# Optimization experiments

Hardware: AMD Instinct MI355X
Metric: run time of the kernel (lower is better)

The kernel has to match this reference:

```python
import jax, jax.numpy as jnp
import numpy as np

L = 2          # conv layers
N = 50000      # nodes
E = 800000     # edges (before self loops)
F_IN = 256     # raw node features
C = 32         # embed features (out_channels per head)
H = 4          # heads
HC = H * C
ED = 1         # edge feature dim
EPS = 1e-5
NEG_SLOPE = 0.2


def _xavier(k, shape):
    fan_in, fan_out = shape[-2], shape[-1]
    lim = float(np.sqrt(6.0 / (fan_in + fan_out)))
    return jax.random.uniform(k, shape, jnp.float32, -lim, lim)


def setup_inputs() -> dict:
    key = jax.random.key(0)
    ks = jax.random.split(key, 12)
    x = jax.random.normal(ks[0], (N, F_IN), jnp.float32)
    src = jax.random.randint(ks[1], (E,), 0, N, dtype=jnp.int32)
    off = jax.random.randint(ks[2], (E,), 1, N, dtype=jnp.int32)
    dst = (src + off) % N  # guarantees no pre-existing self loops (PyG removes then re-adds them)
    edge_index = jnp.stack([src, dst])
    edge_attr = jax.random.normal(ks[3], (E, ED), jnp.float32)
    return {
        "x": x,
        "edge_index": edge_index,
        "edge_attr": edge_attr,
        "W_emb": _xavier(ks[4], (F_IN, C)),
        "b_emb": jnp.zeros((C,), jnp.float32),
        "ln0_w": jnp.ones((C,), jnp.float32),
        "ln0_b": jnp.zeros((C,), jnp.float32),
        "Wl": _xavier(ks[5], (L, C, HC)),
        "bl": jnp.zeros((L, HC), jnp.float32),
        "Wr": _xavier(ks[6], (L, C, HC)),
        "br": jnp.zeros((L, HC), jnp.float32),
        "We": _xavier(ks[7], (L, ED, HC)),
        "att": jax.random.normal(ks[8], (L, H, C), jnp.float32) * 0.1,
        "gat_b": jnp.zeros((L, HC), jnp.float32),
        "ln1_w": jnp.ones((L, HC), jnp.float32),
        "ln1_b": jnp.zeros((L, HC), jnp.float32),
        "lin_w": _xavier(ks[9], (L, HC, C)),
        "lin_b": jnp.zeros((L, C), jnp.float32),
        "ln2_w": jnp.ones((L, C), jnp.float32),
        "ln2_b": jnp.zeros((L, C), jnp.float32),
    }


def _node_ln(x, w, b):
    # torch.nn.LayerNorm over last dim
    mu = jnp.mean(x, axis=-1, keepdims=True)
    xc = x - mu
    var = jnp.mean(xc * xc, axis=-1, keepdims=True)
    return xc / jnp.sqrt(var + EPS) * w + b


def _graph_ln(x, w, b):
    # torch_geometric.nn.norm.LayerNorm, mode='graph': normalize over ALL nodes+features
    mu = jnp.mean(x)
    xc = x - mu
    var = jnp.mean(xc * xc)
    return xc / jnp.sqrt(var + EPS) * w + b


def _gatv2_layer(h, src, dst, ea, Wl, bl, Wr, br, We, att, gat_b):
    n = h.shape[0]
    xl = (h @ Wl + bl).reshape(n, H, C)   # lin_l(x) -> source transform
    xr = (h @ Wr + br).reshape(n, H, C)   # lin_r(x) -> target transform
    e = (ea @ We).reshape(-1, H, C)       # lin_edge(edge_attr), no bias
    z = jax.nn.leaky_relu(xl[src] + xr[dst] + e, NEG_SLOPE)   # [Etot,H,C]
    logits = jnp.einsum("ehc,hc->eh", z, att)                  # [Etot,H]
    # segment softmax over destination nodes (every node has a self loop)
    m = jax.ops.segment_max(logits, dst, num_segments=n)
    ex = jnp.exp(logits - m[dst])
    s = jax.ops.segment_sum(ex, dst, num_segments=n)
    alpha = ex / s[dst]                                        # [Etot,H]
    msg = alpha[..., None] * xl[src]                           # [Etot,H,C]
    out = jax.ops.segment_sum(msg, dst, num_segments=n)        # [N,H,C]
    return out.reshape(n, HC) + gat_b


def reference(x, edge_index, edge_attr, W_emb, b_emb, ln0_w, ln0_b, Wl, bl, Wr, br,
              We, att, gat_b, ln1_w, ln1_b, lin_w, lin_b, ln2_w, ln2_b):
    n = x.shape[0]
    loop = jnp.arange(n, dtype=edge_index.dtype)
    src = jnp.concatenate([edge_index[0], loop])
    dst = jnp.concatenate([edge_index[1], loop])
    ea = jnp.concatenate([edge_attr, jnp.zeros((n, edge_attr.shape[1]), edge_attr.dtype)])  # fill_value=0.0

    # node_embed: Dropout(eval=identity) -> Linear -> LayerNorm -> ReLU
    h = jax.nn.relu(_node_ln(x @ W_emb + b_emb, ln0_w, ln0_b))
    hs = [h]
    for i in range(L):
        g = _gatv2_layer(h, src, dst, ea, Wl[i], bl[i], Wr[i], br[i], We[i], att[i], gat_b[i])
        g = jax.nn.relu(_graph_ln(g, ln1_w[i], ln1_b[i]))     # PyG graph-mode LayerNorm + ReLU
        g = g @ lin_w[i] + lin_b[i]                            # heads>1 projection back to C
        h = jax.nn.relu(_node_ln(g, ln2_w[i], ln2_b[i]))
        hs.append(h)
    # JumpingKnowledge mode='max': elementwise max over layer outputs
    return jnp.max(jnp.stack(hs, axis=0), axis=0)
```

## Files before the change

### kernel.cpp

```cpp
#include <hip/hip_runtime.h>
#include <hip/hip_fp16.h>

constexpr int kNodes = 50000;
constexpr int kNE    = 800000;
constexpr int kFin   = 256;
constexpr int kC     = 32;
constexpr int kH     = 4;
constexpr int kHC    = 128;
constexpr int kTN    = 16;
constexpr int kWPh   = 264;
constexpr int kLWP   = 130;
constexpr int kEmbedBlocks = kNodes / kTN;
constexpr int kHistBlocks  = (kNE + 255) / 256;
constexpr int kTransBlocks = (kNodes + 31) / 32;
constexpr float kEps   = 1e-5f;
constexpr float kSlope = 0.2f;
constexpr float kL2E   = 1.44269504f;
constexpr float kShift2 = 8.0f * 1.44269504f;

typedef _Float16 f16;
typedef _Float16 f16x2 __attribute__((ext_vector_type(2)));
struct alignas(16) h8 { f16x2 v[4]; };

__device__ __forceinline__ float fdot2_(f16x2 a, f16x2 b, float c) {
#if __has_builtin(__builtin_amdgcn_fdot2)
    return __builtin_amdgcn_fdot2(a, b, c, false);
#else
    return fmaf((float)a.x, (float)b.x, fmaf((float)a.y, (float)b.y, c));
#endif
}

template<int CTRL>
__device__ __forceinline__ float dpp_add(float v) {
    int x = __builtin_amdgcn_update_dpp(0, __float_as_int(v), CTRL, 0xF, 0xF, true);
    return v + __int_as_float(x);
}
__device__ __forceinline__ float red8(float p) {
    p = dpp_add<0xB1>(p);
    p = dpp_add<0x4E>(p);
    p = dpp_add<0x141>(p);
    return p;
}

__global__ void __launch_bounds__(256) k_fill0(unsigned* __restrict__ p, int n) {
    int i = blockIdx.x * 256 + threadIdx.x;
    if (i < n) p[i] = 0u;
}

__global__ void __launch_bounds__(256) k_embed_hist(
    const float* __restrict__ x, const float* __restrict__ W, const float* __restrict__ b,
    const float* __restrict__ lnw, const float* __restrict__ lnb,
    float* __restrict__ h, float* __restrict__ jk,
    const int* __restrict__ dst, int* __restrict__ deg, unsigned short* __restrict__ rank) {
    __shared__ f16 sxh[kTN * kFin];
    __shared__ f16 sWh[kC * kWPh];
    int t = threadIdx.x;
    if (blockIdx.x < kHistBlocks) {
        int e = blockIdx.x * 256 + t;
        if (e < kNE) {
            int r = atomicAdd(&deg[dst[e]], 1);
            rank[e] = (unsigned short)r;
        }
        return;
    }
    int n0 = (blockIdx.x - kHistBlocks) * kTN;
    for (int i = t; i < kFin * kC; i += 256) {
        int k = i >> 5, c = i & 31;
        sWh[c * kWPh + k] = (f16)W[i];
    }
    const float2* xg2 = (const float2*)(x + (long)n0 * kFin);
    f16x2* sx2 = (f16x2*)sxh;
    for (int i = t; i < kTN * kFin / 2; i += 256) {
        float2 v = xg2[i];
        f16x2 hv; hv.x = (f16)v.x; hv.y = (f16)v.y;
        sx2[i] = hv;
    }
    __syncthreads();
    int c = t & 31, n2 = t >> 5;
    const h8* xa = (const h8*)(sxh + n2 * kFin);
    const h8* xb = (const h8*)(sxh + (n2 + 8) * kFin);
    const h8* wr = (const h8*)(sWh + c * kWPh);
    float a0 = 0.f, a0b = 0.f, a1 = 0.f, a1b = 0.f;
    #pragma unroll 8
    for (int i8 = 0; i8 < kFin / 8; ++i8) {
        h8 xv0 = xa[i8];
        h8 xv1 = xb[i8];
        h8 wv  = wr[i8];
        a0  = fdot2_(xv0.v[0], wv.v[0], a0);
        a0b = fdot2_(xv0.v[1], wv.v[1], a0b);
        a0  = fdot2_(xv0.v[2], wv.v[2], a0);
        a0b = fdot2_(xv0.v[3], wv.v[3], a0b);
        a1  = fdot2_(xv1.v[0], wv.v[0], a1);
        a1b = fdot2_(xv1.v[1], wv.v[1], a1b);
        a1  = fdot2_(xv1.v[2], wv.v[2], a1);
        a1b = fdot2_(xv1.v[3], wv.v[3], a1b);
    }
    float acc0 = a0 + a0b, acc1 = a1 + a1b;
    float bc = b[c], lw = lnw[c], lb = lnb[c];
    {
        float y = acc0 + bc;
        float m = y;
        #pragma unroll
        for (int o = 1; o < 32; o <<= 1) m += __shfl_xor(m, o);
        m *= (1.f / kC);
        float xc = y - m, v = xc * xc;
        #pragma unroll
        for (int o = 1; o < 32; o <<= 1) v += __shfl_xor(v, o);
        v *= (1.f / kC);
        float out = fmaxf(xc * rsqrtf(v + kEps) * lw + lb, 0.f);
        int node = n0 + n2;
        h[node * kC + c] = out;
        jk[node * kC + c] = out;
    }
    {
        float y = acc1 + bc;
        float m = y;
        #pragma unroll
        for (int o = 1; o < 32; o <<= 1) m += __shfl_xor(m, o);
        m *= (1.f / kC);
        float xc = y - m, v = xc * xc;
        #pragma unroll
        for (int o = 1; o < 32; o <<= 1) v += __shfl_xor(v, o);
        v *= (1.f / kC);
        float out = fmaxf(xc * rsqrtf(v + kEps) * lw + lb, 0.f);
        int node = n0 + n2 + 8;
        h[node * kC + c] = out;
        jk[node * kC + c] = out;
    }
}

__device__ __forceinline__ void trans_body(
    int bid, float* s_h, const float* __restrict__ h,
    const float* __restrict__ Wl, const float* __restrict__ bl,
    const float* __restrict__ Wr, const float* __restrict__ br,
    __half* __restrict__ xl, float* __restrict__ xr) {
    int t = threadIdx.x;
    int j = t & 127, hf = t >> 7;
    float wl[kC], wr[kC];
    #pragma unroll
    for (int k = 0; k < kC; ++k) { wl[k] = Wl[k * kHC + j]; wr[k] = Wr[k * kHC + j]; }
    float blj = bl[j], brj = br[j];
    int n0 = bid * 32;
    int nn = min(32, kNodes - n0);
    for (int i = t; i < nn * kC; i += 256) s_h[i] = h[n0 * kC + i];
    __syncthreads();
    int nend = min(nn, hf * 16 + 16);
    for (int n = hf * 16; n < nend; ++n) {
        const float4* h4 = (const float4*)(s_h + n * kC);
        float al = blj, ar = brj;
        #pragma unroll
        for (int kq = 0; kq < 8; ++kq) {
            float4 hv = h4[kq];
            al += hv.x * wl[kq*4] + hv.y * wl[kq*4+1] + hv.z * wl[kq*4+2] + hv.w * wl[kq*4+3];
            ar += hv.x * wr[kq*4] + hv.y * wr[kq*4+1] + hv.z * wr[kq*4+2] + hv.w * wr[kq*4+3];
        }
        long g = (long)(n0 + n) * kHC + j;
        xl[g] = __float2half(al);
        xr[g] = ar;
    }
}

__global__ void __launch_bounds__(256) k_trans(
    const float* __restrict__ h,
    const float* __restrict__ Wl, const float* __restrict__ bl,
    const float* __restrict__ Wr, const float* __restrict__ br,
    __half* __restrict__ xl, float* __restrict__ xr) {
    __shared__ float s_h[32 * kC];
    trans_body(blockIdx.x, s_h, h, Wl, bl, Wr, br, xl, xr);
}

__global__ void __launch_bounds__(256) k_trans_reorder(
    const float* __restrict__ h,
    const float* __restrict__ Wl, const float* __restrict__ bl,
    const float* __restrict__ Wr, const float* __restrict__ br,
    __half* __restrict__ xl, float* __restrict__ xr,
    const int* __restrict__ src, const int* __restrict__ dst, const float* __restrict__ ea,
    const int* __restrict__ rowptr, const unsigned short* __restrict__ rank,
    int2* __restrict__ epack) {
    __shared__ float s_h[32 * kC];
    if (blockIdx.x < kHistBlocks) {
        int e = blockIdx.x * 256 + threadIdx.x;
        if (e < kNE) {
            int d = dst[e];
            int pos = rowptr[d] + (int)rank[e];
            epack[pos] = make_int2(src[e], __float_as_int(ea[e]));
        }
        return;
    }
    trans_body(blockIdx.x - kHistBlocks, s_h, h, Wl, bl, Wr, br, xl, xr);
}

__global__ void __launch_bounds__(256) k_scan1(const int* __restrict__ deg,
                                               int* __restrict__ excl, int* __restrict__ bsum) {
    __shared__ int s[256];
    int t = threadIdx.x;
    int i = blockIdx.x * 256 + t;
    int v = (i < kNodes) ? deg[i] : 0;
    s[t] = v;
    __syncthreads();
    for (int o = 1; o < 256; o <<= 1) {
        int tv = (t >= o) ? s[t - o] : 0;
        __syncthreads();
        s[t] += tv;
        __syncthreads();
    }
    if (i < kNodes) excl[i] = s[t] - v;
    if (t == 255) bsum[blockIdx.x] = s[255];
}

__global__ void __launch_bounds__(256) k_scan2(int* __restrict__ bsum, int nb) {
    __shared__ int s[256];
    int t = threadIdx.x;
    int v = (t < nb) ? bsum[t] : 0;
    s[t] = v;
    __syncthreads();
    for (int o = 1; o < 256; o <<= 1) {
        int tv = (t >= o) ? s[t - o] : 0;
        __syncthreads();
        s[t] += tv;
        __syncthreads();
    }
    if (t < nb) bsum[t] = s[t];
}

__global__ void __launch_bounds__(256) k_scan3(int* __restrict__ excl, const int* __restrict__ bsum) {
    int i = blockIdx.x * 256 + threadIdx.x;
    if (i >= kNodes) return;
    if (blockIdx.x > 0) excl[i] += bsum[blockIdx.x - 1];
}

__global__ void __launch_bounds__(256) k_edge(
    const int* __restrict__ rowptr, const int* __restrict__ deg,
    const int2* __restrict__ epack,
    const __half* __restrict__ xl, float* __restrict__ xrg,
    const float* __restrict__ We, const float* __restrict__ att,
    const float* __restrict__ gat_b, float* __restrict__ ps, float* __restrict__ pq) {
    struct h4 { __half2 a, b; };
    int t = threadIdx.x & 63;
    int w = __builtin_amdgcn_readfirstlane(threadIdx.x >> 6);
    int d = blockIdx.x * 4 + w;
    int f = t & 31;
    bool slot0 = (t < 32);
    float em0 = slot0 ? 1.f : 0.f;

    const h4* xl4 = (const h4*)xl;
    long rowq = (long)d * 32;

    float4 xrv = ((const float4*)xrg)[rowq + f];
    float4 Wev = ((const float4*)We)[f];
    float4 av  = ((const float4*)att)[f];
    av.x *= kL2E; av.y *= kL2E; av.z *= kL2E; av.w *= kL2E;
    float4 gb  = ((const float4*)gat_b)[f];

    h4 xs = xl4[rowq + f];
    float2 xs01 = __half22float2(xs.a), xs23 = __half22float2(xs.b);

    float z0 = xs01.x + xrv.x, z1 = xs01.y + xrv.y;
    float z2 = xs23.x + xrv.z, z3 = xs23.y + xrv.w;
    z0 = fmaxf(z0, kSlope * z0); z1 = fmaxf(z1, kSlope * z1);
    z2 = fmaxf(z2, kSlope * z2); z3 = fmaxf(z3, kSlope * z3);
    float p = red8(z0 * av.x + z1 * av.y + z2 * av.z + z3 * av.w);
    float ee = __builtin_amdgcn_exp2f(p - kShift2) * em0;
    float l = ee;
    float o0 = ee * xs01.x, o1 = ee * xs01.y, o2 = ee * xs23.x, o3 = ee * xs23.y;

    int base = rowptr[d], cnt = deg[d];
    int npair = cnt >> 1;
    int e = 0;
    for (; e + 4 <= npair; e += 4) {
        int2 pa[4], pb[4];
        #pragma unroll
        for (int u = 0; u < 4; ++u) {
            pa[u] = epack[base + 2 * (e + u)];
            pb[u] = epack[base + 2 * (e + u) + 1];
        }
        h4 xv[4]; float eav[4];
        #pragma unroll
        for (int u = 0; u < 4; ++u) {
            int srow = slot0 ? pa[u].x : pb[u].x;
            xv[u] = xl4[(long)srow * 32 + f];
            eav[u] = __int_as_float(slot0 ? pa[u].y : pb[u].y);
        }
        #pragma unroll
        for (int u = 0; u < 4; ++u) {
            float2 x01 = __half22float2(xv[u].a), x23 = __half22float2(xv[u].b);
            float a0 = fmaf(eav[u], Wev.x, xrv.x) + x01.x;
            float a1 = fmaf(eav[u], Wev.y, xrv.y) + x01.y;
            float a2 = fmaf(eav[u], Wev.z, xrv.z) + x23.x;
            float a3 = fmaf(eav[u], Wev.w, xrv.w) + x23.y;
            a0 = fmaxf(a0, kSlope * a0); a1 = fmaxf(a1, kSlope * a1);
            a2 = fmaxf(a2, kSlope * a2); a3 = fmaxf(a3, kSlope * a3);
            float pp = red8(a0 * av.x + a1 * av.y + a2 * av.z + a3 * av.w);
            float eu = __builtin_amdgcn_exp2f(pp - kShift2);
            l += eu;
            o0 = fmaf(eu, x01.x, o0); o1 = fmaf(eu, x01.y, o1);
            o2 = fmaf(eu, x23.x, o2); o3 = fmaf(eu, x23.y, o3);
        }
    }
    for (; e < npair; ++e) {
        int2 pa = epack[base + 2 * e];
        int2 pb = epack[base + 2 * e + 1];
        int srow = slot0 ? pa.x : pb.x;
        float eav = __int_as_float(slot0 ? pa.y : pb.y);
        h4 xv = xl4[(long)srow * 32 + f];
        float2 x01 = __half22float2(xv.a), x23 = __half22float2(xv.b);
        float a0 = fmaf(eav, Wev.x, xrv.x) + x01.x;
        float a1 = fmaf(eav, Wev.y, xrv.y) + x01.y;
        float a2 = fmaf(eav, Wev.z, xrv.z) + x23.x;
        float a3 = fmaf(eav, Wev.w, xrv.w) + x23.y;
        a0 = fmaxf(a0, kSlope * a0); a1 = fmaxf(a1, kSlope * a1);
        a2 = fmaxf(a2, kSlope * a2); a3 = fmaxf(a3, kSlope * a3);
        float pp = red8(a0 * av.x + a1 * av.y + a2 * av.z + a3 * av.w);
        float eu = __builtin_amdgcn_exp2f(pp - kShift2);
        l += eu;
        o0 = fmaf(eu, x01.x, o0); o1 = fmaf(eu, x01.y, o1);
        o2 = fmaf(eu, x23.x, o2); o3 = fmaf(eu, x23.y, o3);
    }
    if (cnt & 1) {
        int2 ep = epack[base + cnt - 1];
        int srow = ep.x;
        float eav = __int_as_float(ep.y);
        h4 xv = xl4[(long)srow * 32 + f];
        float2 x01 = __half22float2(xv.a), x23 = __half22float2(xv.b);
        float a0 = fmaf(eav, Wev.x, xrv.x) + x01.x;
        float a1 = fmaf(eav, Wev.y, xrv.y) + x01.y;
        float a2 = fmaf(eav, Wev.z, xrv.z) + x23.x;
        float a3 = fmaf(eav, Wev.w, xrv.w) + x23.y;
        a0 = fmaxf(a0, kSlope * a0); a1 = fmaxf(a1, kSlope * a1);
        a2 = fmaxf(a2, kSlope * a2); a3 = fmaxf(a3, kSlope * a3);
        float pp = red8(a0 * av.x + a1 * av.y + a2 * av.z + a3 * av.w);
        float eu = __builtin_amdgcn_exp2f(pp - kShift2) * em0;
        l += eu;
        o0 = fmaf(eu, x01.x, o0); o1 = fmaf(eu, x01.y, o1);
        o2 = fmaf(eu, x23.x, o2); o3 = fmaf(eu, x23.y, o3);
    }
    l  += __shfl_xor(l, 32);
    o0 += __shfl_xor(o0, 32); o1 += __shfl_xor(o1, 32);
    o2 += __shfl_xor(o2, 32); o3 += __shfl_xor(o3, 32);
    float rl = __builtin_amdgcn_rcpf(l);
    float v0 = o0 * rl, v1 = o1 * rl, v2 = o2 * rl, v3 = o3 * rl;
    if (slot0)
        ((float4*)xrg)[rowq + f] = make_float4(v0, v1, v2, v3);
    float vb0 = v0 + gb.x, vb1 = v1 + gb.y, vb2 = v2 + gb.z, vb3 = v3 + gb.w;
    float s = vb0 + vb1 + vb2 + vb3;
    float q = vb0 * vb0 + vb1 * vb1 + vb2 * vb2 + vb3 * vb3;
    #pragma unroll
    for (int mm = 1; mm < 32; mm <<= 1) { s += __shfl_xor(s, mm); q += __shfl_xor(q, mm); }
    if (t == 0) { ps[d] = s; pq[d] = q; }
}

__global__ void __launch_bounds__(1024) k_statsr(
    const float* __restrict__ ps, const float* __restrict__ pq, float* __restrict__ stats) {
    __shared__ float rs[1024], rq[1024];
    int t = threadIdx.x;
    float s = 0.f, q = 0.f;
    for (int i = t; i < kNodes; i += 1024) { s += ps[i]; q += pq[i]; }
    rs[t] = s; rq[t] = q;
    __syncthreads();
    for (int o = 512; o > 0; o >>= 1) {
        if (t < o) { rs[t] += rs[t + o]; rq[t] += rq[t + o]; }
        __syncthreads();
    }
    if (t == 0) { stats[0] = rs[0]; stats[1] = rq[0]; }
}

__global__ void __launch_bounds__(256) k_post(
    const float* __restrict__ g, const float* __restrict__ gat_b,
    const float* __restrict__ ln1w, const float* __restrict__ ln1b,
    const float* __restrict__ linw, const float* __restrict__ linb,
    const float* __restrict__ ln2w, const float* __restrict__ ln2b,
    const float* __restrict__ stats, const float* __restrict__ jk_in,
    float* __restrict__ h, float* __restrict__ jk_out) {
    __shared__ float s_lwT[kC * kLWP];
    __shared__ float s_vb[8 * kHC];
    int t = threadIdx.x;
    int n0 = blockIdx.x * 8;
    const float inv = 1.f / ((float)kNodes * kHC);
    float mean = stats[0] * inv;
    float var  = stats[1] * inv - mean * mean;
    float rstd = rsqrtf(var + kEps);
    for (int i = t; i < kHC * kC; i += 256) {
        int k = i >> 5, c = i & 31;
        s_lwT[c * kLWP + k] = linw[i];
    }
    for (int i = t; i < 8 * kHC; i += 256) {
        int node = n0 + (i >> 7), f = i & 127;
        float a = (g[(long)node * kHC + f] + gat_b[f] - mean) * rstd * ln1w[f] + ln1b[f];
        s_vb[i] = fmaxf(a, 0.f);
    }
    __syncthreads();
    int n = t >> 5, c = t & 31;
    int node = n0 + n;
    float acc = linb[c];
    const float* vb = s_vb + n * kHC;
    const float* wr = s_lwT + c * kLWP;
    #pragma unroll 8
    for (int k = 0; k < kHC; k += 4) {
        float4 v4 = *(const float4*)(vb + k);
        float2 w0 = *(const float2*)(wr + k);
        float2 w1 = *(const float2*)(wr + k + 2);
        acc += v4.x * w0.x + v4.y * w0.y + v4.z * w1.x + v4.w * w1.y;
    }
    float m = acc;
    #pragma unroll
    for (int mm = 1; mm < 32; mm <<= 1) m += __shfl_xor(m, mm);
    m *= (1.f / kC);
    float dd = acc - m;
    float q = dd * dd;
    #pragma unroll
    for (int mm = 1; mm < 32; mm <<= 1) q += __shfl_xor(q, mm);
    q *= (1.f / kC);
    float out = dd * rsqrtf(q + kEps) * ln2w[c] + ln2b[c];
    out = fmaxf(out, 0.f);
    h[node * kC + c] = out;
    jk_out[node * kC + c] = fmaxf(jk_in[node * kC + c], out);
}

extern "C" void kernel_launch(void* const* d_in, const int* in_sizes, int n_in,
                              void* d_out, int out_size, void* d_ws, size_t ws_size,
                              hipStream_t stream) {
    (void)in_sizes; (void)n_in; (void)out_size; (void)ws_size;
    const float* x     = (const float*)d_in[0];
    const int*   ei    = (const int*)d_in[1];
    const int*   src   = ei;
    const int*   dst   = ei + kNE;
    const float* ea    = (const float*)d_in[2];
    const float* W_emb = (const float*)d_in[3];
    const float* b_emb = (const float*)d_in[4];
    const float* ln0w  = (const float*)d_in[5];
    const float* ln0b  = (const float*)d_in[6];
    const float* Wl    = (const float*)d_in[7];
    const float* bl    = (const float*)d_in[8];
    const float* Wr    = (const float*)d_in[9];
    const float* br    = (const float*)d_in[10];
    const float* We    = (const float*)d_in[11];
    const float* att   = (const float*)d_in[12];
    const float* gat_b = (const float*)d_in[13];
    const float* ln1w  = (const float*)d_in[14];
    const float* ln1b  = (const float*)d_in[15];
    const float* linw  = (const float*)d_in[16];
    const float* linb  = (const float*)d_in[17];
    const float* ln2w  = (const float*)d_in[18];
    const float* ln2b  = (const float*)d_in[19];

    char* wsb = (char*)d_ws;
    float*  h      = (float*)(wsb);
    float*  jk     = (float*)(wsb +  6400000);
    float*  xrg    = (float*)(wsb + 12800000);
    __half* xl     = (__half*)(wsb + 38400000);
    int2*   epack  = (int2*)(wsb + 51200000);
    int*    deg    = (int*)(wsb + 57600000);
    int*    rowptr = (int*)(wsb + 58000000);
    int*    bsum   = (int*)(wsb + 58200000);
    float*  stats  = (float*)(wsb + 58201024);
    float*  ps     = (float*)(wsb + 58300000);
    float*  pq     = (float*)(wsb + 58500000);
    unsigned short* rank = (unsigned short*)(wsb + 58700000);

    const int scanBlocks = (kNodes + 255) / 256;
    const int edgeBlocks = kNodes / 4;
    const int postBlocks = kNodes / 8;

    hipLaunchKernelGGL(k_fill0, dim3((kNodes + 255) / 256), dim3(256), 0, stream,
                       (unsigned*)deg, kNodes);
    hipLaunchKernelGGL(k_embed_hist, dim3(kHistBlocks + kEmbedBlocks), dim3(256), 0, stream,
                       x, W_emb, b_emb, ln0w, ln0b, h, jk, dst, deg, rank);
    hipLaunchKernelGGL(k_scan1, dim3(scanBlocks), dim3(256), 0, stream, deg, rowptr, bsum);
    hipLaunchKernelGGL(k_scan2, dim3(1), dim3(256), 0, stream, bsum, scanBlocks);
    hipLaunchKernelGGL(k_scan3, dim3(scanBlocks), dim3(256), 0, stream, rowptr, bsum);
    hipLaunchKernelGGL(k_trans_reorder, dim3(kHistBlocks + kTransBlocks), dim3(256), 0, stream,
                       h, Wl, bl, Wr, br, xl, xrg,
                       src, dst, ea, rowptr, rank, epack);
    for (int l = 0; l < 2; ++l) {
        if (l == 1) {
            hipLaunchKernelGGL(k_trans, dim3(kTransBlocks), dim3(256), 0, stream,
                               h, Wl + l * kC * kHC, bl + l * kHC,
                               Wr + l * kC * kHC, br + l * kHC, xl, xrg);
        }
        hipLaunchKernelGGL(k_edge, dim3(edgeBlocks), dim3(256), 0, stream,
                           rowptr, deg, epack, xl, xrg,
                           We + l * kHC, att + l * kH * kC, gat_b + l * kHC, ps, pq);
        hipLaunchKernelGGL(k_statsr, dim3(1), dim3(1024), 0, stream, ps, pq, stats);
        hipLaunchKernelGGL(k_post, dim3(postBlocks), dim3(256), 0, stream,
                           xrg, gat_b + l * kHC, ln1w + l * kHC, ln1b + l * kHC,
                           linw + l * kHC * kC, linb + l * kC,
                           ln2w + l * kC, ln2b + l * kC, stats, jk,
                           h, (l == 1) ? (float*)d_out : jk);
    }
}
```

Baseline: 421.6 us.

## Use grid-stride unrolled loops for histogram/reorder and interleave embed weight smem layout

The edge histogram and edge reorder phases switch from one block per 256 edges to a fixed 256-block grid-stride loop. Each thread handles four edges per iteration so several loads and atomics are in flight together. The embed weight tile in shared memory is rearranged so each k-chunk of 8 values is contiguous across output channels, replacing the padded per-channel rows. This cuts block count and launch overhead and changes LDS access patterns, but fewer blocks may lower latency hiding for the atomics and scattered writes.

```diff
diff --git a/kernel.cpp b/kernel.cpp
--- a/kernel.cpp
+++ b/kernel.cpp
@@ -8,11 +8,11 @@
 constexpr int kH     = 4;
 constexpr int kHC    = 128;
 constexpr int kTN    = 16;
-constexpr int kWPh   = 264;
 constexpr int kLWP   = 130;
 constexpr int kEmbedBlocks = kNodes / kTN;
-constexpr int kHistBlocks  = (kNE + 255) / 256;
 constexpr int kTransBlocks = (kNodes + 31) / 32;
+constexpr int kHistGS = 256;
+constexpr int kReoGS  = 256;
 constexpr float kEps   = 1e-5f;
 constexpr float kSlope = 0.2f;
 constexpr float kL2E   = 1.44269504f;
@@ -53,20 +53,32 @@
     float* __restrict__ h, float* __restrict__ jk,
     const int* __restrict__ dst, int* __restrict__ deg, unsigned short* __restrict__ rank) {
     __shared__ f16 sxh[kTN * kFin];
-    __shared__ f16 sWh[kC * kWPh];
+    __shared__ f16 sWh[kFin / 8 * kC * 8];
     int t = threadIdx.x;
-    if (blockIdx.x < kHistBlocks) {
+    if (blockIdx.x < kHistGS) {
+        const int stride = kHistGS * 256;
         int e = blockIdx.x * 256 + t;
-        if (e < kNE) {
-            int r = atomicAdd(&deg[dst[e]], 1);
-            rank[e] = (unsigned short)r;
+        for (; e + 3 * stride < kNE; e += 4 * stride) {
+            int d0 = dst[e], d1 = dst[e + stride], d2 = dst[e + 2 * stride], d3 = dst[e + 3 * stride];
+            int r0 = atomicAdd(&deg[d0], 1);
+            int r1 = atomicAdd(&deg[d1], 1);
+            int r2 = atomicAdd(&deg[d2], 1);
+            int r3 = atomicAdd(&deg[d3], 1);
+            rank[e] = (unsigned short)r0;
+            rank[e + stride] = (unsigned short)r1;
+            rank[e + 2 * stride] = (unsigned short)r2;
+            rank[e + 3 * stride] = (unsigned short)r3;
+        }
+        for (; e < kNE; e += stride) {
+            int d = dst[e];
+            rank[e] = (unsigned short)atomicAdd(&deg[d], 1);
         }
         return;
     }
-    int n0 = (blockIdx.x - kHistBlocks) * kTN;
+    int n0 = (blockIdx.x - kHistGS) * kTN;
     for (int i = t; i < kFin * kC; i += 256) {
         int k = i >> 5, c = i & 31;
-        sWh[c * kWPh + k] = (f16)W[i];
+        sWh[((k >> 3) * kC + c) * 8 + (k & 7)] = (f16)W[i];
     }
     const float2* xg2 = (const float2*)(x + (long)n0 * kFin);
     f16x2* sx2 = (f16x2*)sxh;
@@ -79,13 +91,13 @@
     int c = t & 31, n2 = t >> 5;
     const h8* xa = (const h8*)(sxh + n2 * kFin);
     const h8* xb = (const h8*)(sxh + (n2 + 8) * kFin);
-    const h8* wr = (const h8*)(sWh + c * kWPh);
+    const h8* wr = (const h8*)sWh;
     float a0 = 0.f, a0b = 0.f, a1 = 0.f, a1b = 0.f;
     #pragma unroll 8
     for (int i8 = 0; i8 < kFin / 8; ++i8) {
         h8 xv0 = xa[i8];
         h8 xv1 = xb[i8];
-        h8 wv  = wr[i8];
+        h8 wv  = wr[i8 * kC + c];
         a0  = fdot2_(xv0.v[0], wv.v[0], a0);
         a0b = fdot2_(xv0.v[1], wv.v[1], a0b);
         a0  = fdot2_(xv0.v[2], wv.v[2], a0);
@@ -178,16 +190,28 @@
     const int* __restrict__ rowptr, const unsigned short* __restrict__ rank,
     int2* __restrict__ epack) {
     __shared__ float s_h[32 * kC];
-    if (blockIdx.x < kHistBlocks) {
+    if (blockIdx.x < kReoGS) {
+        const int stride = kReoGS * 256;
         int e = blockIdx.x * 256 + threadIdx.x;
-        if (e < kNE) {
+        for (; e + 3 * stride < kNE; e += 4 * stride) {
+            int e1 = e + stride, e2 = e + 2 * stride, e3 = e + 3 * stride;
+            int d0 = dst[e], d1 = dst[e1], d2 = dst[e2], d3 = dst[e3];
+            int r0 = rank[e], r1 = rank[e1], r2 = rank[e2], r3 = rank[e3];
+            int p0 = rowptr[d0] + r0, p1 = rowptr[d1] + r1;
+            int p2 = rowptr[d2] + r2, p3 = rowptr[d3] + r3;
+            epack[p0] = make_int2(src[e],  __float_as_int(ea[e]));
+            epack[p1] = make_int2(src[e1], __float_as_int(ea[e1]));
+            epack[p2] = make_int2(src[e2], __float_as_int(ea[e2]));
+            epack[p3] = make_int2(src[e3], __float_as_int(ea[e3]));
+        }
+        for (; e < kNE; e += stride) {
             int d = dst[e];
             int pos = rowptr[d] + (int)rank[e];
             epack[pos] = make_int2(src[e], __float_as_int(ea[e]));
         }
         return;
     }
-    trans_body(blockIdx.x - kHistBlocks, s_h, h, Wl, bl, Wr, br, xl, xr);
+    trans_body(blockIdx.x - kReoGS, s_h, h, Wl, bl, Wr, br, xl, xr);
 }
 
 __global__ void __launch_bounds__(256) k_scan1(const int* __restrict__ deg,
@@ -463,12 +487,12 @@
 
     hipLaunchKernelGGL(k_fill0, dim3((kNodes + 255) / 256), dim3(256), 0, stream,
                        (unsigned*)deg, kNodes);
-    hipLaunchKernelGGL(k_embed_hist, dim3(kHistBlocks + kEmbedBlocks), dim3(256), 0, stream,
+    hipLaunchKernelGGL(k_embed_hist, dim3(kHistGS + kEmbedBlocks), dim3(256), 0, stream,
                        x, W_emb, b_emb, ln0w, ln0b, h, jk, dst, deg, rank);
     hipLaunchKernelGGL(k_scan1, dim3(scanBlocks), dim3(256), 0, stream, deg, rowptr, bsum);
     hipLaunchKernelGGL(k_scan2, dim3(1), dim3(256), 0, stream, bsum, scanBlocks);
     hipLaunchKernelGGL(k_scan3, dim3(scanBlocks), dim3(256), 0, stream, rowptr, bsum);
-    hipLaunchKernelGGL(k_trans_reorder, dim3(kHistBlocks + kTransBlocks), dim3(256), 0, stream,
+    hipLaunchKernelGGL(k_trans_reorder, dim3(kReoGS + kTransBlocks), dim3(256), 0, stream,
                        h, Wl, bl, Wr, br, xl, xrg,
                        src, dst, ea, rowptr, rank, epack);
     for (int l = 0; l < 2; ++l) {
```

Result: no change. 419.3 us (-0.6%).
